# Performance work log

Hardware: AMD Instinct MI355X
Metric: run time of the kernel (lower is better)

## Reference

```python
import jax, jax.numpy as jnp
import numpy as np

BS, T, F, H, YIN = 32, 64, 32, 256, 10


def setup_inputs() -> dict:
    key = jax.random.key(0)
    ks = jax.random.split(key, 20)
    s = 0.1
    rn = lambda k, shape: jax.random.normal(k, shape, dtype=jnp.float32) * s
    return {
        'Y': jax.random.normal(ks[0], (BS, T, YIN), dtype=jnp.float32),
        'X_p': jax.random.normal(ks[1], (BS, T, F), dtype=jnp.float32),
        'X_n': jax.random.normal(ks[2], (BS, T, F), dtype=jnp.float32),
        # Y-stream LSTM (input 10)
        'Wy': rn(ks[3], (YIN, 4 * H)), 'Uy': rn(ks[4], (H, 4 * H)), 'by': jnp.zeros((4 * H,), jnp.float32),
        # per-feature single-input LSTM banks (F independent LSTMs, input size 1)
        'Wxp': rn(ks[5], (F, 4 * H)), 'Uxp': rn(ks[6], (F, H, 4 * H)), 'bxp': jnp.zeros((F, 4 * H), jnp.float32),
        'Wxn': rn(ks[7], (F, 4 * H)), 'Uxn': rn(ks[8], (F, H, 4 * H)), 'bxn': jnp.zeros((F, 4 * H), jnp.float32),
        # MI-LSTM: main stream gates (i,f,g,o), aux streams (gate, candidate) each
        'Wm': rn(ks[9], (H, 4 * H)), 'Um': rn(ks[10], (H, 4 * H)), 'bm': jnp.zeros((4 * H,), jnp.float32),
        'Wpa': rn(ks[11], (H, 2 * H)), 'Upa': rn(ks[12], (H, 2 * H)), 'bpa': jnp.zeros((2 * H,), jnp.float32),
        'Wna': rn(ks[13], (H, 2 * H)), 'Una': rn(ks[14], (H, 2 * H)), 'bna': jnp.zeros((2 * H,), jnp.float32),
        'Wa': rn(ks[15], (H, H)), 'ba': jnp.zeros((H,), jnp.float32),
        # temporal attention + output head
        'Watt': rn(ks[16], (H, H)), 'batt': jnp.zeros((H,), jnp.float32), 'vatt': rn(ks[17], (H,)),
        'Wlin': rn(ks[18], (H, 1)), 'blin': jnp.zeros((1,), jnp.float32),
    }


def _lstm(x, W, U, b):
    # standard LSTM; x: [bs,T,in] -> hidden sequence [bs,T,H]
    xg = jnp.einsum('bti,ig->btg', x, W) + b  # precompute input projections
    bs, h = x.shape[0], U.shape[0]

    def step(carry, g_t):
        hh, cc = carry
        g = g_t + hh @ U
        i, f, gg, o = jnp.split(g, 4, axis=-1)
        i, f, o = jax.nn.sigmoid(i), jax.nn.sigmoid(f), jax.nn.sigmoid(o)
        cc = f * cc + i * jnp.tanh(gg)
        hh = o * jnp.tanh(cc)
        return (hh, cc), hh

    init = (jnp.zeros((bs, h), x.dtype), jnp.zeros((bs, h), x.dtype))
    _, hs = jax.lax.scan(step, init, jnp.swapaxes(xg, 0, 1))
    return jnp.swapaxes(hs, 0, 1)


def _feature_lstms(x, W, U, b):
    # F independent input-size-1 LSTMs batched into one scan; returns the mean
    # over features of their hidden sequences (= torch.mean(torch.stack(...),0)).
    # x: [bs,T,F], W: [F,4H], U: [F,H,4H], b: [F,4H] -> [bs,T,H]
    xg = x[..., None] * W + b  # [bs,T,F,4H]
    bs, f, h = x.shape[0], W.shape[0], U.shape[1]

    def step(carry, g_t):
        hh, cc = carry  # [bs,F,H]
        g = g_t + jnp.einsum('bfh,fhg->bfg', hh, U)
        i, fg, gg, o = jnp.split(g, 4, axis=-1)
        i, fg, o = jax.nn.sigmoid(i), jax.nn.sigmoid(fg), jax.nn.sigmoid(o)
        cc = fg * cc + i * jnp.tanh(gg)
        hh = o * jnp.tanh(cc)
        return (hh, cc), jnp.mean(hh, axis=1)  # mean over feature-LSTMs

    init = (jnp.zeros((bs, f, h), x.dtype), jnp.zeros((bs, f, h), x.dtype))
    _, hs = jax.lax.scan(step, init, jnp.swapaxes(xg, 0, 1))
    return jnp.swapaxes(hs, 0, 1)


def _milstm(y, p, n, Wm, Um, bm, Wpa, Upa, bpa, Wna, Una, bna, Wa, ba):
    # Multi-input LSTM: main stream y with full i/f/g/o gates; aux streams p,n
    # contribute gated candidates; cell-state attention mixes the 3 candidates.
    yg = jnp.einsum('bth,hg->btg', y, Wm) + bm
    pg = jnp.einsum('bth,hg->btg', p, Wpa) + bpa
    ng = jnp.einsum('bth,hg->btg', n, Wna) + bna
    bs, h = y.shape[0], Um.shape[0]

    def step(carry, gs):
        hh, cc = carry
        yg_t, pg_t, ng_t = gs
        g = yg_t + hh @ Um
        i, f, gy, o = jnp.split(g, 4, axis=-1)
        i, f, o = jax.nn.sigmoid(i), jax.nn.sigmoid(f), jax.nn.sigmoid(o)
        gp = pg_t + hh @ Upa
        ip, cp = jnp.split(gp, 2, axis=-1)
        gn = ng_t + hh @ Una
        inn, cn = jnp.split(gn, 2, axis=-1)
        l = jnp.stack([i * jnp.tanh(gy),
                       jax.nn.sigmoid(ip) * jnp.tanh(cp),
                       jax.nn.sigmoid(inn) * jnp.tanh(cn)], axis=1)  # [bs,3,H]
        att = jnp.tanh(cc @ Wa + ba)  # [bs,H]
        alpha = jax.nn.softmax(jnp.einsum('bkh,bh->bk', l, att), axis=-1)
        ltilde = jnp.einsum('bk,bkh->bh', alpha, l)
        cc = f * cc + ltilde
        hh = o * jnp.tanh(cc)
        return (hh, cc), hh

    init = (jnp.zeros((bs, h), y.dtype), jnp.zeros((bs, h), y.dtype))
    xs = (jnp.swapaxes(yg, 0, 1), jnp.swapaxes(pg, 0, 1), jnp.swapaxes(ng, 0, 1))
    _, hs = jax.lax.scan(step, init, xs)
    return jnp.swapaxes(hs, 0, 1)


def reference(Y, X_p, X_n, Wy, Uy, by, Wxp, Uxp, bxp, Wxn, Uxn, bxn,
              Wm, Um, bm, Wpa, Upa, bpa, Wna, Una, bna, Wa, ba,
              Watt, batt, vatt, Wlin, blin):
    Yh = _lstm(Y, Wy, Uy, by)                      # Y_tilde_hidden [bs,T,H]
    Ph = _feature_lstms(X_p, Wxp, Uxp, bxp)        # P_tilde [bs,T,H]
    Nh = _feature_lstms(X_n, Wxn, Uxn, bxn)        # N_tilde [bs,T,H]
    Hm = _milstm(Yh, Ph, Nh, Wm, Um, bm, Wpa, Upa, bpa, Wna, Una, bna, Wa, ba)
    # temporal additive attention
    s = jnp.einsum('bth,h->bt', jnp.tanh(jnp.einsum('bth,hg->btg', Hm, Watt) + batt), vatt)
    alpha = jax.nn.softmax(s, axis=-1)
    ytilde = jnp.einsum('bt,bth->bh', alpha, Hm)
    return jax.nn.relu(ytilde @ Wlin + blin)       # [bs,1]
```

## Files before the change

### kernel.cpp

```cpp
#include <hip/hip_runtime.h>
#include <math.h>

#define T 64
#define H 256

typedef _Float16 f16;
typedef _Float16 f16x8 __attribute__((ext_vector_type(8)));
typedef float f32x4 __attribute__((ext_vector_type(4)));

__device__ __forceinline__ float sigm(float x) { return 1.f / (1.f + __expf(-x)); }
__device__ __forceinline__ float ftanh(float x) { return 1.f - 2.f / (__expf(2.f * x) + 1.f); }

__global__ __launch_bounds__(256) void k_prep_u(
    const float* __restrict__ Uxp, const float* __restrict__ Uxn,
    const float* __restrict__ Uy, f16* __restrict__ Uf2)
{
  __shared__ f16 lds[32][1024];
  const int tid = threadIdx.x;
  const int lstm = blockIdx.x >> 3, kt = blockIdx.x & 7;
  const float* src = (lstm < 32) ? (Uxp + (size_t)lstm * 262144)
                   : (lstm < 64) ? (Uxn + (size_t)(lstm - 32) * 262144)
                   : Uy;
  const int k0 = kt * 32;
  for (int i = tid; i < 32 * 1024; i += 256) {
    const int row = i >> 10, col = i & 1023;
    lds[row][col] = (f16)src[(size_t)(k0 + row) * 1024 + col];
  }
  __syncthreads();
  const int l = tid & 63, c0 = tid >> 6;
  for (int c = c0; c < 64; c += 4) {
    const int w = c >> 3, ct = c & 7, g = ct >> 1, nt = ct & 1;
    f16x8 v;
    #pragma unroll
    for (int e = 0; e < 8; ++e)
      v[e] = lds[(l >> 4) * 8 + e][g * 256 + w * 32 + nt * 16 + (l & 15)];
    *(f16x8*)(Uf2 + (((((size_t)lstm * 8 + w) * 8 + kt) * 8 + ct) * 64 + l) * 8) = v;
  }
}

__global__ __launch_bounds__(64) void k_prep_wmi(
    const float* __restrict__ Um, const float* __restrict__ Upa,
    const float* __restrict__ Una, const float* __restrict__ Wa,
    f16* __restrict__ Wmi)
{
  const int l = threadIdx.x;
  const int c = blockIdx.x * 2 + (l >> 5);
  const int kc = l & 31;
  const float* src; int scol, ld;
  if (c < 1024)      { src = Um;  scol = c;        ld = 1024; }
  else if (c < 1536) { src = Upa; scol = c - 1024; ld = 512;  }
  else if (c < 2048) { src = Una; scol = c - 1536; ld = 512;  }
  else               { src = Wa;  scol = c - 2048; ld = 256;  }
  f16x8 v;
  #pragma unroll
  for (int e = 0; e < 8; ++e) v[e] = (f16)src[(size_t)(kc * 8 + e) * ld + scol];
  *(f16x8*)(Wmi + ((size_t)kc * 2304 + c) * 8) = v;
}

__global__ __launch_bounds__(512) void k_prep_x(
    const float* __restrict__ Xp, const float* __restrict__ Xn, float* __restrict__ Xt)
{
  const int s = blockIdx.x >> 5, f = blockIdx.x & 31;
  const float* X = s ? Xn : Xp;
  for (int i = threadIdx.x; i < 2048; i += 512) {
    const int t = i >> 5, b = i & 31;
    Xt[((size_t)(s * 32 + f) * 64 + t) * 32 + b] = X[((size_t)b * 64 + t) * 32 + f];
  }
}

__global__ __launch_bounds__(1024) void k_prep_yg0(
    const float* __restrict__ Y, const float* __restrict__ Wy,
    const float* __restrict__ by, float* __restrict__ yg0t)
{
  const int t = blockIdx.x, col = threadIdx.x;
  float wv[10];
  #pragma unroll
  for (int i = 0; i < 10; ++i) wv[i] = Wy[i * 1024 + col];
  const float bv = by[col];
  for (int b = 0; b < 32; ++b) {
    float a = bv;
    #pragma unroll
    for (int i = 0; i < 10; ++i) a += Y[((size_t)b * 64 + t) * 10 + i] * wv[i];
    yg0t[((size_t)t * 1024 + col) * 32 + b] = a;
  }
}

__global__ __launch_bounds__(512, 2) void k_scan(
    const float* __restrict__ Xt,
    const float* __restrict__ Wxp, const float* __restrict__ bxp,
    const float* __restrict__ Wxn, const float* __restrict__ bxn,
    const f16* __restrict__ Uf2, const float* __restrict__ yg0t,
    float* __restrict__ Yh, f16* __restrict__ hseq)
{
  __shared__ __align__(16) f16 hfrag[2 * 8 * 64 * 8];
  const int tid = threadIdx.x;
  const int w = tid >> 6, l = tid & 63;
  const int cl = l & 15, lq = l >> 4;
  const int lstm = blockIdx.x;
  const bool isY = (lstm == 64);
  const int s = (lstm >= 32 && !isY) ? 1 : 0;
  const int f = lstm & 31;

  const f16* UB = Uf2 + ((size_t)(lstm * 8 + w) * 64) * 512 + (size_t)l * 8;

  float Wc[4][2], Bc[4][2];
  const float* xrow = nullptr;
  if (!isY) {
    const float* Wf = (s ? Wxn : Wxp) + (size_t)f * 1024;
    const float* bf = (s ? bxn : bxp) + (size_t)f * 1024;
    #pragma unroll
    for (int g = 0; g < 4; ++g)
      #pragma unroll
      for (int nt = 0; nt < 2; ++nt) {
        const int col = g * 256 + w * 32 + nt * 16 + cl;
        Wc[g][nt] = Wf[col]; Bc[g][nt] = bf[col];
      }
    xrow = Xt + (size_t)(s * 32 + f) * 2048;
  }
  f16* hout = hseq + (size_t)lstm * (64 * 32 * 256);

  float c[2][2][4];
  #pragma unroll
  for (int nt = 0; nt < 2; ++nt)
    #pragma unroll
    for (int mt = 0; mt < 2; ++mt)
      #pragma unroll
      for (int j = 0; j < 4; ++j) c[nt][mt][j] = 0.f;

  for (int i = tid; i < 1024; i += 512) ((uint4*)hfrag)[i] = uint4{0, 0, 0, 0};
  __syncthreads();

  for (int t = 0; t < T; ++t) {
    f16x8 Uc[8], Un[8];
    #pragma unroll
    for (int ct = 0; ct < 8; ++ct) Uc[ct] = *(const f16x8*)(UB + ct * 512);

    f32x4 acc[8][2];
    #pragma unroll
    for (int ct = 0; ct < 8; ++ct) { acc[ct][0] = f32x4{0,0,0,0}; acc[ct][1] = f32x4{0,0,0,0}; }

    #pragma unroll
    for (int kt = 0; kt < 8; ++kt) {
      if (kt < 7) {
        #pragma unroll
        for (int ct = 0; ct < 8; ++ct)
          Un[ct] = *(const f16x8*)(UB + ((kt + 1) * 8 + ct) * 512);
      }
      const f16x8 a0 = *(const f16x8*)(hfrag + (0 * 8 + kt) * 512 + l * 8);
      const f16x8 a1 = *(const f16x8*)(hfrag + (1 * 8 + kt) * 512 + l * 8);
      #pragma unroll
      for (int ct = 0; ct < 8; ++ct) {
        acc[ct][0] = __builtin_amdgcn_mfma_f32_16x16x32_f16(a0, Uc[ct], acc[ct][0], 0, 0, 0);
        acc[ct][1] = __builtin_amdgcn_mfma_f32_16x16x32_f16(a1, Uc[ct], acc[ct][1], 0, 0, 0);
      }
      #pragma unroll
      for (int ct = 0; ct < 8; ++ct) Uc[ct] = Un[ct];
    }
    __syncthreads();

    #pragma unroll
    for (int mt = 0; mt < 2; ++mt) {
      float4 xq;
      if (!isY) xq = *(const float4*)(xrow + t * 32 + mt * 16 + lq * 4);
      #pragma unroll
      for (int nt = 0; nt < 2; ++nt) {
        float4 yq[4];
        if (isY) {
          #pragma unroll
          for (int g = 0; g < 4; ++g) {
            const int col = g * 256 + w * 32 + nt * 16 + cl;
            yq[g] = *(const float4*)(yg0t + ((size_t)t * 1024 + col) * 32 + mt * 16 + lq * 4);
          }
        }
        const int n = w * 32 + nt * 16 + cl;
        #pragma unroll
        for (int j = 0; j < 4; ++j) {
          const int b = mt * 16 + lq * 4 + j;
          float p0, p1, p2, p3;
          if (isY) {
            p0 = acc[0 * 2 + nt][mt][j] + ((const float*)&yq[0])[j];
            p1 = acc[1 * 2 + nt][mt][j] + ((const float*)&yq[1])[j];
            p2 = acc[2 * 2 + nt][mt][j] + ((const float*)&yq[2])[j];
            p3 = acc[3 * 2 + nt][mt][j] + ((const float*)&yq[3])[j];
          } else {
            const float x = ((const float*)&xq)[j];
            p0 = acc[0 * 2 + nt][mt][j] + x * Wc[0][nt] + Bc[0][nt];
            p1 = acc[1 * 2 + nt][mt][j] + x * Wc[1][nt] + Bc[1][nt];
            p2 = acc[2 * 2 + nt][mt][j] + x * Wc[2][nt] + Bc[2][nt];
            p3 = acc[3 * 2 + nt][mt][j] + x * Wc[3][nt] + Bc[3][nt];
          }
          const float ig = sigm(p0), fg = sigm(p1), gy = ftanh(p2), og = sigm(p3);
          c[nt][mt][j] = fg * c[nt][mt][j] + ig * gy;
          const float h = og * ftanh(c[nt][mt][j]);
          const int lanep = (lq * 4 + j) + (nt * 2 + (cl >> 3)) * 16;
          hfrag[(mt * 8 + w) * 512 + lanep * 8 + (cl & 7)] = (f16)h;
          if (isY) Yh[((size_t)b * T + t) * H + n] = h;
          else hout[(((size_t)t * 32 + b) * 256) + n] = (f16)h;
        }
      }
    }
    __syncthreads();
  }
}

__global__ __launch_bounds__(256) void k_mean(
    const f16* __restrict__ hseq, float* __restrict__ Ph, float* __restrict__ Nh)
{
  const int bt = blockIdx.x;
  const int b = bt >> 6, t = bt & 63;
  const int n = threadIdx.x;
  const size_t base = (((size_t)t * 32 + b) * 256) + n;
  float s0 = 0.f, s1 = 0.f;
  #pragma unroll
  for (int f = 0; f < 32; ++f) {
    s0 += (float)hseq[(size_t)f        * (64 * 32 * 256) + base];
    s1 += (float)hseq[(size_t)(f + 32) * (64 * 32 * 256) + base];
  }
  Ph[(size_t)bt * 256 + n] = s0 * 0.03125f;
  Nh[(size_t)bt * 256 + n] = s1 * 0.03125f;
}

__global__ __launch_bounds__(1024) void k_xg(
    const float* __restrict__ Yh, const float* __restrict__ Ph, const float* __restrict__ Nh,
    const float* __restrict__ Wm, const float* __restrict__ bm,
    const float* __restrict__ Wpa, const float* __restrict__ bpa,
    const float* __restrict__ Wna, const float* __restrict__ bna,
    float* __restrict__ yg, float* __restrict__ pg, float* __restrict__ ng)
{
  __shared__ __align__(16) float A[8][768];
  const int tid = threadIdx.x;
  const int ro  = blockIdx.x * 8;

  for (int idx = tid; idx < 8 * 768; idx += 1024) {
    const int r = idx / 768, cc = idx % 768;
    const int row = ro + r;
    float v;
    if (cc < 256)      v = Yh[(size_t)row * H + cc];
    else if (cc < 512) v = Ph[(size_t)row * H + (cc - 256)];
    else               v = Nh[(size_t)row * H + (cc - 512)];
    A[r][cc] = v;
  }
  __syncthreads();

  float acc[8];
  #pragma unroll
  for (int r = 0; r < 8; ++r) acc[r] = bm[tid];
  for (int k = 0; k < H; k += 4) {
    const float w0 = Wm[(k + 0) * 1024 + tid];
    const float w1 = Wm[(k + 1) * 1024 + tid];
    const float w2 = Wm[(k + 2) * 1024 + tid];
    const float w3 = Wm[(k + 3) * 1024 + tid];
    #pragma unroll
    for (int r = 0; r < 8; ++r) {
      const float4 av = *(const float4*)&A[r][k];
      acc[r] += w0 * av.x + w1 * av.y + w2 * av.z + w3 * av.w;
    }
  }
  #pragma unroll
  for (int r = 0; r < 8; ++r) yg[(size_t)(ro + r) * 1024 + tid] = acc[r];

  const int col = tid & 511;
  const float* Wx = (tid < 512) ? Wpa : Wna;
  const float* bx = (tid < 512) ? bpa : bna;
  float* outp     = (tid < 512) ? pg : ng;
  const int aoff  = (tid < 512) ? 256 : 512;
  #pragma unroll
  for (int r = 0; r < 8; ++r) acc[r] = bx[col];
  for (int k = 0; k < H; k += 4) {
    const float w0 = Wx[(k + 0) * 512 + col];
    const float w1 = Wx[(k + 1) * 512 + col];
    const float w2 = Wx[(k + 2) * 512 + col];
    const float w3 = Wx[(k + 3) * 512 + col];
    #pragma unroll
    for (int r = 0; r < 8; ++r) {
      const float4 av = *(const float4*)&A[r][aoff + k];
      acc[r] += w0 * av.x + w1 * av.y + w2 * av.z + w3 * av.w;
    }
  }
  #pragma unroll
  for (int r = 0; r < 8; ++r) outp[(size_t)(ro + r) * 512 + col] = acc[r];
}

__global__ __launch_bounds__(1024, 1) void k_mi(
    const float* __restrict__ yg, const float* __restrict__ pg, const float* __restrict__ ng,
    const f16* __restrict__ Wmi, const float* __restrict__ ba,
    float* __restrict__ Hm)
{
  __shared__ float g_all[2304];
  __shared__ __align__(16) f16 h_lds[256];
  __shared__ __align__(16) f16 c_lds[256];
  __shared__ float red[3][4];
  const int tid = threadIdx.x;
  const int b = blockIdx.x;

  if (tid < 256) { h_lds[tid] = (f16)0.f; c_lds[tid] = (f16)0.f; }
  const float bav = (tid < 256) ? ba[tid] : 0.f;
  float creg = 0.f;
  __syncthreads();

  for (int t = 0; t < T; ++t) {
    const size_t row = (size_t)b * T + t;

    float pre[8];
    if (tid < 256) {
      #pragma unroll
      for (int g = 0; g < 4; ++g) pre[g] = yg[row * 1024 + g * 256 + tid];
      pre[4] = pg[row * 512 + tid];       pre[5] = pg[row * 512 + 256 + tid];
      pre[6] = ng[row * 512 + tid];       pre[7] = ng[row * 512 + 256 + tid];
    }

    for (int c = tid; c < 2304; c += 1024) {
      const f16* hsrc = (c >= 2048) ? c_lds : h_lds;
      const f16* wcol = Wmi + (size_t)c * 8;
      float acc = 0.f;
      #pragma unroll 8
      for (int kc = 0; kc < 32; ++kc) {
        const f16x8 wv = *(const f16x8*)(wcol + (size_t)kc * 2304 * 8);
        const f16x8 hv = *(const f16x8*)(hsrc + kc * 8);
        #pragma unroll
        for (int e = 0; e < 8; ++e) acc += (float)wv[e] * (float)hv[e];
      }
      g_all[c] = acc;
    }
    __syncthreads();

    float l0 = 0.f, l1 = 0.f, l2 = 0.f, fg = 0.f, og = 0.f;
    if (tid < 256) {
      const int n = tid;
      const float gi = sigm(g_all[n]            + pre[0]);
      fg             = sigm(g_all[256 + n]      + pre[1]);
      const float gy = ftanh(g_all[512 + n]     + pre[2]);
      og             = sigm(g_all[768 + n]      + pre[3]);
      const float ip = sigm(g_all[1024 + n]     + pre[4]);
      const float cp = ftanh(g_all[1280 + n]    + pre[5]);
      const float in = sigm(g_all[1536 + n]     + pre[6]);
      const float cn = ftanh(g_all[1792 + n]    + pre[7]);
      const float att = ftanh(g_all[2048 + n]   + bav);
      l0 = gi * gy; l1 = ip * cp; l2 = in * cn;
      float v0 = l0 * att, v1 = l1 * att, v2 = l2 * att;
      #pragma unroll
      for (int off = 32; off; off >>= 1) {
        v0 += __shfl_down(v0, off);
        v1 += __shfl_down(v1, off);
        v2 += __shfl_down(v2, off);
      }
      if ((tid & 63) == 0) {
        red[0][tid >> 6] = v0; red[1][tid >> 6] = v1; red[2][tid >> 6] = v2;
      }
    }
    __syncthreads();

    if (tid < 256) {
      const int n = tid;
      const float s0 = red[0][0] + red[0][1] + red[0][2] + red[0][3];
      const float s1 = red[1][0] + red[1][1] + red[1][2] + red[1][3];
      const float s2 = red[2][0] + red[2][1] + red[2][2] + red[2][3];
      const float m  = fmaxf(s0, fmaxf(s1, s2));
      const float e0 = __expf(s0 - m), e1 = __expf(s1 - m), e2 = __expf(s2 - m);
      const float lt = (e0 * l0 + e1 * l1 + e2 * l2) / (e0 + e1 + e2);
      creg = fg * creg + lt;
      const float h = og * ftanh(creg);
      h_lds[n] = (f16)h;
      c_lds[n] = (f16)creg;
      Hm[row * H + n] = h;
    }
    __syncthreads();
  }
}

__global__ __launch_bounds__(256) void k_att(
    const float* __restrict__ Hm, const float* __restrict__ Watt, const float* __restrict__ batt,
    const float* __restrict__ vatt, const float* __restrict__ Wlin, const float* __restrict__ blin,
    float* __restrict__ out)
{
  __shared__ __align__(16) float hm8[8][H];
  __shared__ float vred[8][4];
  __shared__ float s_lds[T];
  __shared__ float alpha_lds[T];
  __shared__ float red4[4];
  const int n = threadIdx.x;
  const int b = blockIdx.x;
  const float bn = batt[n], vn = vatt[n];

  for (int t0 = 0; t0 < T; t0 += 8) {
    __syncthreads();
    #pragma unroll
    for (int r = 0; r < 8; ++r) hm8[r][n] = Hm[((size_t)b * T + t0 + r) * H + n];
    __syncthreads();
    float acc[8];
    #pragma unroll
    for (int r = 0; r < 8; ++r) acc[r] = bn;
    for (int k = 0; k < H; k += 4) {
      const float w0 = Watt[(k + 0) * H + n];
      const float w1 = Watt[(k + 1) * H + n];
      const float w2 = Watt[(k + 2) * H + n];
      const float w3 = Watt[(k + 3) * H + n];
      #pragma unroll
      for (int r = 0; r < 8; ++r) {
        const float4 hv = *(const float4*)&hm8[r][k];
        acc[r] += w0 * hv.x + w1 * hv.y + w2 * hv.z + w3 * hv.w;
      }
    }
    #pragma unroll
    for (int r = 0; r < 8; ++r) {
      float v = tanhf(acc[r]) * vn;
      for (int off = 32; off; off >>= 1) v += __shfl_down(v, off);
      if ((n & 63) == 0) vred[r][n >> 6] = v;
    }
    __syncthreads();
    if (n < 8) s_lds[t0 + n] = vred[n][0] + vred[n][1] + vred[n][2] + vred[n][3];
  }
  __syncthreads();

  if (n < T) {
    const float sv = s_lds[n];
    float m = sv;
    for (int off = 32; off; off >>= 1) m = fmaxf(m, __shfl_xor(m, off));
    const float e = expf(sv - m);
    float sum = e;
    for (int off = 32; off; off >>= 1) sum += __shfl_xor(sum, off);
    alpha_lds[n] = e / sum;
  }
  __syncthreads();

  float acc = 0.f;
  for (int t = 0; t < T; ++t) acc += alpha_lds[t] * Hm[((size_t)b * T + t) * H + n];
  float p = acc * Wlin[n];
  for (int off = 32; off; off >>= 1) p += __shfl_down(p, off);
  if ((n & 63) == 0) red4[n >> 6] = p;
  __syncthreads();
  if (n == 0) out[b] = fmaxf(red4[0] + red4[1] + red4[2] + red4[3] + blin[0], 0.f);
}

extern "C" void kernel_launch(void* const* d_in, const int* in_sizes, int n_in,
                              void* d_out, int out_size, void* d_ws, size_t ws_size,
                              hipStream_t stream) {
  const float* Yin  = (const float*)d_in[0];
  const float* Xp   = (const float*)d_in[1];
  const float* Xn   = (const float*)d_in[2];
  const float* Wy   = (const float*)d_in[3];
  const float* Uy   = (const float*)d_in[4];
  const float* by   = (const float*)d_in[5];
  const float* Wxp  = (const float*)d_in[6];
  const float* Uxp  = (const float*)d_in[7];
  const float* bxp  = (const float*)d_in[8];
  const float* Wxn  = (const float*)d_in[9];
  const float* Uxn  = (const float*)d_in[10];
  const float* bxn  = (const float*)d_in[11];
  const float* Wm   = (const float*)d_in[12];
  const float* Um   = (const float*)d_in[13];
  const float* bm   = (const float*)d_in[14];
  const float* Wpa  = (const float*)d_in[15];
  const float* Upa  = (const float*)d_in[16];
  const float* bpa  = (const float*)d_in[17];
  const float* Wna  = (const float*)d_in[18];
  const float* Una  = (const float*)d_in[19];
  const float* bna  = (const float*)d_in[20];
  const float* Wa   = (const float*)d_in[21];
  const float* ba   = (const float*)d_in[22];
  const float* Watt = (const float*)d_in[23];
  const float* batt = (const float*)d_in[24];
  const float* vatt = (const float*)d_in[25];
  const float* Wlin = (const float*)d_in[26];
  const float* blin = (const float*)d_in[27];

  float* ws = (float*)d_ws;
  float*    Yh    = ws;
  float*    Ph    = ws + 524288;
  float*    Nh    = ws + 1048576;
  float*    Hm    = ws + 1572864;
  float*    yg    = ws + 2097152;
  float*    pg    = ws + 4194304;
  float*    ng    = ws + 5242880;
  float*    yg0t  = ws + 6291456;
  float*    Xt    = ws + 8388608;
  f16*      Uf2   = (f16*)(ws + 8519680);
  f16*      Wmi   = (f16*)(ws + 17039360);
  f16*      hseq  = (f16*)(ws + 17334272);
  float*    out   = (float*)d_out;

  k_prep_u   <<<520, 256, 0, stream>>>(Uxp, Uxn, Uy, Uf2);
  k_prep_wmi <<<1152, 64, 0, stream>>>(Um, Upa, Una, Wa, Wmi);
  k_prep_x   <<<64, 512, 0, stream>>>(Xp, Xn, Xt);
  k_prep_yg0 <<<64, 1024, 0, stream>>>(Yin, Wy, by, yg0t);

  k_scan<<<65, 512, 0, stream>>>(Xt, Wxp, bxp, Wxn, bxn, Uf2, yg0t, Yh, hseq);
  k_mean<<<2048, 256, 0, stream>>>(hseq, Ph, Nh);
  k_xg  <<<256, 1024, 0, stream>>>(Yh, Ph, Nh, Wm, bm, Wpa, bpa, Wna, bna, yg, pg, ng);
  k_mi  <<<32, 1024, 0, stream>>>(yg, pg, ng, Wmi, ba, Hm);
  k_att <<<32, 256, 0, stream>>>(Hm, Watt, batt, vatt, Wlin, blin, out);
}
```

Before: 2.374 ms.

## Split LSTM scan columns across 16 waves with 1024-thread blocks

Each k_scan block now runs 16 waves instead of 8, and each wave owns 16 hidden columns instead of 32. The U weight repack is changed to match, so every wave handles 4 gate tiles per k-step instead of 8. The aim is to halve per-wave MFMA work and register pressure on the serial 64-step recurrence, giving more latency hiding per CU. The cost is more waves contending on the block-wide barriers and on LDS, with only one block per CU.

```diff
diff --git a/kernel.cpp b/kernel.cpp
--- a/kernel.cpp
+++ b/kernel.cpp
@@ -28,13 +28,13 @@
   }
   __syncthreads();
   const int l = tid & 63, c0 = tid >> 6;
-  for (int c = c0; c < 64; c += 4) {
-    const int w = c >> 3, ct = c & 7, g = ct >> 1, nt = ct & 1;
+  for (int fc = c0; fc < 64; fc += 4) {
+    const int w = fc >> 2, g = fc & 3;
     f16x8 v;
     #pragma unroll
     for (int e = 0; e < 8; ++e)
-      v[e] = lds[(l >> 4) * 8 + e][g * 256 + w * 32 + nt * 16 + (l & 15)];
-    *(f16x8*)(Uf2 + (((((size_t)lstm * 8 + w) * 8 + kt) * 8 + ct) * 64 + l) * 8) = v;
+      v[e] = lds[(l >> 4) * 8 + e][g * 256 + w * 16 + (l & 15)];
+    *(f16x8*)(Uf2 + (((((size_t)lstm * 16 + w) * 8 + kt) * 4 + g) * 64 + l) * 8) = v;
   }
 }
 
@@ -85,7 +85,7 @@
   }
 }
 
-__global__ __launch_bounds__(512, 2) void k_scan(
+__global__ __launch_bounds__(1024, 1) void k_scan(
     const float* __restrict__ Xt,
     const float* __restrict__ Wxp, const float* __restrict__ bxp,
     const float* __restrict__ Wxn, const float* __restrict__ bxn,
@@ -100,103 +100,97 @@
   const bool isY = (lstm == 64);
   const int s = (lstm >= 32 && !isY) ? 1 : 0;
   const int f = lstm & 31;
-
-  const f16* UB = Uf2 + ((size_t)(lstm * 8 + w) * 64) * 512 + (size_t)l * 8;
-
-  float Wc[4][2], Bc[4][2];
+  const int n = w * 16 + cl;
+
+  const f16* UB = Uf2 + ((size_t)(lstm * 16 + w) * 32) * 512 + (size_t)l * 8;
+
+  float Wc[4], Bc[4];
   const float* xrow = nullptr;
   if (!isY) {
     const float* Wf = (s ? Wxn : Wxp) + (size_t)f * 1024;
     const float* bf = (s ? bxn : bxp) + (size_t)f * 1024;
     #pragma unroll
-    for (int g = 0; g < 4; ++g)
-      #pragma unroll
-      for (int nt = 0; nt < 2; ++nt) {
-        const int col = g * 256 + w * 32 + nt * 16 + cl;
-        Wc[g][nt] = Wf[col]; Bc[g][nt] = bf[col];
-      }
+    for (int g = 0; g < 4; ++g) { Wc[g] = Wf[g * 256 + n]; Bc[g] = bf[g * 256 + n]; }
     xrow = Xt + (size_t)(s * 32 + f) * 2048;
   }
   f16* hout = hseq + (size_t)lstm * (64 * 32 * 256);
 
-  float c[2][2][4];
-  #pragma unroll
-  for (int nt = 0; nt < 2; ++nt)
-    #pragma unroll
-    for (int mt = 0; mt < 2; ++mt)
-      #pragma unroll
-      for (int j = 0; j < 4; ++j) c[nt][mt][j] = 0.f;
-
-  for (int i = tid; i < 1024; i += 512) ((uint4*)hfrag)[i] = uint4{0, 0, 0, 0};
-  __syncthreads();
+  float c[2][4];
+  #pragma unroll
+  for (int mt = 0; mt < 2; ++mt)
+    #pragma unroll
+    for (int j = 0; j < 4; ++j) c[mt][j] = 0.f;
+
+  ((uint4*)hfrag)[tid] = uint4{0, 0, 0, 0};
+  __syncthreads();
+
+  const int wkt   = n >> 5;
+  const int lanehi = ((n >> 3) & 3) * 16;
+  const int we    = n & 7;
 
   for (int t = 0; t < T; ++t) {
-    f16x8 Uc[8], Un[8];
-    #pragma unroll
-    for (int ct = 0; ct < 8; ++ct) Uc[ct] = *(const f16x8*)(UB + ct * 512);
-
-    f32x4 acc[8][2];
-    #pragma unroll
-    for (int ct = 0; ct < 8; ++ct) { acc[ct][0] = f32x4{0,0,0,0}; acc[ct][1] = f32x4{0,0,0,0}; }
+    f32x4 acc[4][2];
+    #pragma unroll
+    for (int g = 0; g < 4; ++g) { acc[g][0] = f32x4{0,0,0,0}; acc[g][1] = f32x4{0,0,0,0}; }
+
+    f16x8 Uc[4];
+    #pragma unroll
+    for (int g = 0; g < 4; ++g) Uc[g] = *(const f16x8*)(UB + g * 512);
 
     #pragma unroll
     for (int kt = 0; kt < 8; ++kt) {
+      f16x8 Un[4];
       if (kt < 7) {
         #pragma unroll
-        for (int ct = 0; ct < 8; ++ct)
-          Un[ct] = *(const f16x8*)(UB + ((kt + 1) * 8 + ct) * 512);
+        for (int g = 0; g < 4; ++g)
+          Un[g] = *(const f16x8*)(UB + ((kt + 1) * 4 + g) * 512);
       }
       const f16x8 a0 = *(const f16x8*)(hfrag + (0 * 8 + kt) * 512 + l * 8);
       const f16x8 a1 = *(const f16x8*)(hfrag + (1 * 8 + kt) * 512 + l * 8);
       #pragma unroll
-      for (int ct = 0; ct < 8; ++ct) {
-        acc[ct][0] = __builtin_amdgcn_mfma_f32_16x16x32_f16(a0, Uc[ct], acc[ct][0], 0, 0, 0);
-        acc[ct][1] = __builtin_amdgcn_mfma_f32_16x16x32_f16(a1, Uc[ct], acc[ct][1], 0, 0, 0);
-      }
-      #pragma unroll
-      for (int ct = 0; ct < 8; ++ct) Uc[ct] = Un[ct];
+      for (int g = 0; g < 4; ++g) {
+        acc[g][0] = __builtin_amdgcn_mfma_f32_16x16x32_f16(a0, Uc[g], acc[g][0], 0, 0, 0);
+        acc[g][1] = __builtin_amdgcn_mfma_f32_16x16x32_f16(a1, Uc[g], acc[g][1], 0, 0, 0);
+      }
+      #pragma unroll
+      for (int g = 0; g < 4; ++g) Uc[g] = Un[g];
     }
     __syncthreads();
 
     #pragma unroll
     for (int mt = 0; mt < 2; ++mt) {
       float4 xq;
-      if (!isY) xq = *(const float4*)(xrow + t * 32 + mt * 16 + lq * 4);
-      #pragma unroll
-      for (int nt = 0; nt < 2; ++nt) {
-        float4 yq[4];
+      float4 yq[4];
+      if (!isY) {
+        xq = *(const float4*)(xrow + t * 32 + mt * 16 + lq * 4);
+      } else {
+        #pragma unroll
+        for (int g = 0; g < 4; ++g)
+          yq[g] = *(const float4*)(yg0t + ((size_t)t * 1024 + g * 256 + n) * 32 + mt * 16 + lq * 4);
+      }
+      #pragma unroll
+      for (int j = 0; j < 4; ++j) {
+        const int b = mt * 16 + lq * 4 + j;
+        float p0, p1, p2, p3;
         if (isY) {
-          #pragma unroll
-          for (int g = 0; g < 4; ++g) {
-            const int col = g * 256 + w * 32 + nt * 16 + cl;
-            yq[g] = *(const float4*)(yg0t + ((size_t)t * 1024 + col) * 32 + mt * 16 + lq * 4);
-          }
+          p0 = acc[0][mt][j] + ((const float*)&yq[0])[j];
+          p1 = acc[1][mt][j] + ((const float*)&yq[1])[j];
+          p2 = acc[2][mt][j] + ((const float*)&yq[2])[j];
+          p3 = acc[3][mt][j] + ((const float*)&yq[3])[j];
+        } else {
+          const float x = ((const float*)&xq)[j];
+          p0 = acc[0][mt][j] + x * Wc[0] + Bc[0];
+          p1 = acc[1][mt][j] + x * Wc[1] + Bc[1];
+          p2 = acc[2][mt][j] + x * Wc[2] + Bc[2];
+          p3 = acc[3][mt][j] + x * Wc[3] + Bc[3];
         }
-        const int n = w * 32 + nt * 16 + cl;
-        #pragma unroll
-        for (int j = 0; j < 4; ++j) {
-          const int b = mt * 16 + lq * 4 + j;
-          float p0, p1, p2, p3;
-          if (isY) {
-            p0 = acc[0 * 2 + nt][mt][j] + ((const float*)&yq[0])[j];
-            p1 = acc[1 * 2 + nt][mt][j] + ((const float*)&yq[1])[j];
-            p2 = acc[2 * 2 + nt][mt][j] + ((const float*)&yq[2])[j];
-            p3 = acc[3 * 2 + nt][mt][j] + ((const float*)&yq[3])[j];
-          } else {
-            const float x = ((const float*)&xq)[j];
-            p0 = acc[0 * 2 + nt][mt][j] + x * Wc[0][nt] + Bc[0][nt];
-            p1 = acc[1 * 2 + nt][mt][j] + x * Wc[1][nt] + Bc[1][nt];
-            p2 = acc[2 * 2 + nt][mt][j] + x * Wc[2][nt] + Bc[2][nt];
-            p3 = acc[3 * 2 + nt][mt][j] + x * Wc[3][nt] + Bc[3][nt];
-          }
-          const float ig = sigm(p0), fg = sigm(p1), gy = ftanh(p2), og = sigm(p3);
-          c[nt][mt][j] = fg * c[nt][mt][j] + ig * gy;
-          const float h = og * ftanh(c[nt][mt][j]);
-          const int lanep = (lq * 4 + j) + (nt * 2 + (cl >> 3)) * 16;
-          hfrag[(mt * 8 + w) * 512 + lanep * 8 + (cl & 7)] = (f16)h;
-          if (isY) Yh[((size_t)b * T + t) * H + n] = h;
-          else hout[(((size_t)t * 32 + b) * 256) + n] = (f16)h;
-        }
+        const float ig = sigm(p0), fg = sigm(p1), gy = ftanh(p2), og = sigm(p3);
+        c[mt][j] = fg * c[mt][j] + ig * gy;
+        const float h = og * ftanh(c[mt][j]);
+        const int lanep = (lq * 4 + j) + lanehi;
+        hfrag[(mt * 8 + wkt) * 512 + lanep * 8 + we] = (f16)h;
+        if (isY) Yh[((size_t)b * T + t) * H + n] = h;
+        else hout[(((size_t)t * 32 + b) * 256) + n] = (f16)h;
       }
     }
     __syncthreads();
@@ -484,7 +478,7 @@
   k_prep_x   <<<64, 512, 0, stream>>>(Xp, Xn, Xt);
   k_prep_yg0 <<<64, 1024, 0, stream>>>(Yin, Wy, by, yg0t);
 
-  k_scan<<<65, 512, 0, stream>>>(Xt, Wxp, bxp, Wxn, bxn, Uf2, yg0t, Yh, hseq);
+  k_scan<<<65, 1024, 0, stream>>>(Xt, Wxp, bxp, Wxn, bxn, Uf2, yg0t, Yh, hseq);
   k_mean<<<2048, 256, 0, stream>>>(hseq, Ph, Nh);
   k_xg  <<<256, 1024, 0, stream>>>(Yh, Ph, Nh, Wm, bm, Wpa, bpa, Wna, bna, yg, pg, ng);
   k_mi  <<<32, 1024, 0, stream>>>(yg, pg, ng, Wmi, ba, Hm);
```

Result: no change. 2.354 ms (-0.8%).
